# Performance work log

Measured on AMD Instinct MI355X. Metric: run time of the kernel, lower is better.

Reference implementation:

```python
import jax, jax.numpy as jnp
import numpy as np

HEADS = 4
DIM_HEAD = 32
SCALE = DIM_HEAD ** -0.5
GN_EPS = 1e-5


def setup_inputs() -> dict:
    key = jax.random.key(0)
    k1, k2, k3 = jax.random.split(key, 3)
    dim, hidden = 64, HEADS * DIM_HEAD
    x = jax.random.normal(k1, (2, dim, 32, 32, 32), dtype=jnp.float32)
    w_qkv = jax.random.normal(k2, (3 * hidden, dim), dtype=jnp.float32) * (dim ** -0.5)
    w_out = jax.random.normal(k3, (dim, hidden), dtype=jnp.float32) * (hidden ** -0.5)
    b_out = jnp.zeros((dim,), dtype=jnp.float32)
    gn_w = jnp.ones((dim,), dtype=jnp.float32)
    gn_b = jnp.zeros((dim,), dtype=jnp.float32)
    return {"x": x, "w_qkv": w_qkv, "w_out": w_out, "b_out": b_out, "gn_w": gn_w, "gn_b": gn_b}


def reference(x, w_qkv, w_out, b_out, gn_w, gn_b):
    b, c, D, H, W = x.shape
    n = D * H * W
    xf = x.reshape(b, c, n)  # flatten spatial: 1x1 Conv3d == channel matmul
    qkv = jnp.einsum('oc,bcn->bon', w_qkv, xf)  # [b, 3*hidden, n]
    q, k, v = jnp.split(qkv, 3, axis=1)
    rs = lambda t: t.reshape(b, HEADS, DIM_HEAD, n)  # b h d n
    q, k, v = rs(q), rs(k), rs(v)
    q = jax.nn.softmax(q, axis=2) * SCALE   # softmax over head-dim channels
    k = jax.nn.softmax(k, axis=3)           # softmax over spatial positions
    context = jnp.einsum('bhdn,bhen->bhde', k, v)   # [b, h, d, e], tiny
    out = jnp.einsum('bhde,bhdn->bhen', context, q)  # [b, h, e, n]
    out = out.reshape(b, HEADS * DIM_HEAD, n)
    # to_out: 1x1 Conv3d with bias, then GroupNorm(1, dim)
    y = jnp.einsum('oc,bcn->bon', w_out, out) + b_out[None, :, None]
    mean = jnp.mean(y, axis=(1, 2), keepdims=True)
    var = jnp.var(y, axis=(1, 2), keepdims=True)
    y = (y - mean) * jax.lax.rsqrt(var + GN_EPS)
    y = y * gn_w[None, :, None] + gn_b[None, :, None]
    return y.reshape(b, -1, D, H, W)
```

## Files before the change

### kernel.cpp

```cpp
#include <hip/hip_runtime.h>
#include <hip/hip_bf16.h>

#define NB 2
#define C_IN 64
#define N_SP 32768
#define NHEADS 4
#define DH 32
#define HID 128
#define QK_SCALE 0.17677669529663687f
#define GN_EPS_C 1e-5f
#define NGN 2097152.0f

using bf16x8 = __attribute__((ext_vector_type(8))) short;
using f32x4  = __attribute__((ext_vector_type(4))) float;
using u16x4  = __attribute__((ext_vector_type(4))) unsigned short;
using u16x8  = __attribute__((ext_vector_type(8))) unsigned short;

__device__ __forceinline__ unsigned short f2bf(float f) {
    union { float f; unsigned u; } c{f};
    unsigned r = c.u + 0x7FFFu + ((c.u >> 16) & 1u);
    return (unsigned short)(r >> 16);
}
__device__ __forceinline__ float bf2f(unsigned short u) {
    union { unsigned u; float f; } c{ (unsigned)u << 16 };
    return c.f;
}

__device__ __forceinline__ void load_xf(const float* __restrict__ xb, int n0,
        int lg, int lc, bf16x8 xf[4][2]) {
#pragma unroll
    for (int s = 0; s < 4; ++s) {
        int n = n0 + s * 16 + lc;
#pragma unroll
        for (int kk = 0; kk < 2; ++kk) {
            bf16x8 v;
#pragma unroll
            for (int j = 0; j < 8; ++j)
                v[j] = (short)f2bf(xb[(size_t)(kk * 32 + lg * 8 + j) * N_SP + n]);
            xf[s][kk] = v;
        }
    }
}

__global__ __launch_bounds__(256) void kA(const float* __restrict__ x,
        const float* __restrict__ wqkv,
        float* __restrict__ ctx_part, float* __restrict__ ksum_part) {
    __shared__ unsigned short kt[8192];
    __shared__ unsigned short vt[8192];
    const int t = threadIdx.x, wv = t >> 6, l = t & 63, lg = l >> 4, lc = l & 15;
    const int blk = blockIdx.x;
    const int b = blk >> 7, nblk = blk & 127;
    const int n0 = nblk * 256 + wv * 64;

    bf16x8 xf[4][2];
    load_xf(x + (size_t)b * C_IN * N_SP, n0, lg, lc, xf);

    const int di = wv >> 1, ei = wv & 1;
#pragma unroll
    for (int h = 0; h < NHEADS; ++h) {
        f32x4 ka[4][2] = {}, va[4][2] = {};
#pragma unroll
        for (int e = 0; e < 2; ++e)
#pragma unroll
            for (int kk = 0; kk < 2; ++kk) {
                const float* pk = wqkv + (size_t)(HID + h * 32 + e * 16 + lc) * 64 + kk * 32 + lg * 8;
                const float* pv = wqkv + (size_t)(2 * HID + h * 32 + e * 16 + lc) * 64 + kk * 32 + lg * 8;
                bf16x8 wk, wf;
#pragma unroll
                for (int j = 0; j < 8; ++j) { wk[j] = (short)f2bf(pk[j]); wf[j] = (short)f2bf(pv[j]); }
#pragma unroll
                for (int s = 0; s < 4; ++s) {
                    ka[s][e] = __builtin_amdgcn_mfma_f32_16x16x32_bf16(xf[s][kk], wk, ka[s][e], 0, 0, 0);
                    va[s][e] = __builtin_amdgcn_mfma_f32_16x16x32_bf16(xf[s][kk], wf, va[s][e], 0, 0, 0);
                }
            }
        __syncthreads();
#pragma unroll
        for (int s = 0; s < 4; ++s)
#pragma unroll
            for (int e = 0; e < 2; ++e) {
                u16x4 pk, pv;
#pragma unroll
                for (int r = 0; r < 4; ++r) {
                    pk[r] = f2bf(__expf(ka[s][e][r]));
                    pv[r] = f2bf(va[s][e][r]);
                }
                int ch = e * 16 + lc;
                int pos = wv * 64 + s * 16 + lg * 4;
                int ba = (ch * 512 + pos * 2) ^ ((ch & 7) << 4);
                *(u16x4*)((char*)kt + ba) = pk;
                *(u16x4*)((char*)vt + ba) = pv;
            }
        __syncthreads();
        f32x4 ca = {};
        float ks = 0.f;
#pragma unroll
        for (int k0 = 0; k0 < 256; k0 += 32) {
            int ar = di * 16 + lc, br = ei * 16 + lc;
            bf16x8 af = *(const bf16x8*)((const char*)kt + ((ar * 512 + (k0 + lg * 8) * 2) ^ ((ar & 7) << 4)));
            bf16x8 bf = *(const bf16x8*)((const char*)vt + ((br * 512 + (k0 + lg * 8) * 2) ^ ((br & 7) << 4)));
            if (ei == 0) {
#pragma unroll
                for (int j = 0; j < 8; ++j) ks += bf2f((unsigned short)af[j]);
            }
            ca = __builtin_amdgcn_mfma_f32_16x16x32_bf16(af, bf, ca, 0, 0, 0);
        }
        float* cp = ctx_part + ((size_t)(b * 4 + h) * 128 + nblk) * 1024;
#pragma unroll
        for (int r = 0; r < 4; ++r)
            cp[(di * 16 + lg * 4 + r) * 32 + ei * 16 + lc] = ca[r];
        if (ei == 0) {
            ks += __shfl_xor(ks, 16);
            ks += __shfl_xor(ks, 32);
            if (lg == 0)
                ksum_part[((size_t)(b * 4 + h) * 128 + nblk) * 32 + di * 16 + lc] = ks;
        }
    }
}

__global__ __launch_bounds__(256) void kB(const float* __restrict__ ctx_part,
        const float* __restrict__ ksum_part, const float* __restrict__ wout,
        unsigned short* __restrict__ weff) {
    __shared__ float cred2[2][128];
    __shared__ float cred[128];
    __shared__ float ks2[4][32];
    __shared__ float ksl[4];
    const int blk = blockIdx.x;
    const int g = blk >> 3, ds = blk & 7;
    const int bb = g >> 2, h = g & 3;
    const int t = threadIdx.x;
    const int tt = t & 127, th = t >> 7;
    float a = 0.f;
    const float* cp = ctx_part + ((size_t)g * 128 + th * 64) * 1024 + ds * 128 + tt;
#pragma unroll 8
    for (int i = 0; i < 64; ++i) a += cp[(size_t)i * 1024];
    cred2[th][tt] = a;
    if (t < 128) {
        int dl = t >> 5, ic = t & 31;
        float s = 0.f;
        const float* kp = ksum_part + ((size_t)g * 128 + ic * 4) * 32 + ds * 4 + dl;
#pragma unroll
        for (int i = 0; i < 4; ++i) s += kp[i * 32];
        ks2[dl][ic] = s;
    }
    __syncthreads();
    if (t < 128) cred[t] = cred2[0][t] + cred2[1][t];
    if (t < 4) {
        float s = 0.f;
#pragma unroll
        for (int i = 0; i < 32; ++i) s += ks2[t][i];
        ksl[t] = s;
    }
    __syncthreads();
    const int o = t >> 2, dl = t & 3;
    const float* wrow = wout + o * HID + h * 32;
    const float* crow = cred + dl * 32;
    float acc = 0.f;
#pragma unroll
    for (int e = 0; e < 32; ++e) acc = fmaf(wrow[e], crow[e], acc);
    acc /= ksl[dl];
    weff[((size_t)bb * 64 + o) * 128 + h * 32 + ds * 4 + dl] = f2bf(acc);
}

__global__ __launch_bounds__(256) void kC(const float* __restrict__ x,
        const float* __restrict__ wqkv, const unsigned short* __restrict__ weff,
        const float* __restrict__ bout, unsigned short* __restrict__ y_t,
        float* __restrict__ pstats) {
    __shared__ unsigned short qt[256 * 128];
    __shared__ float red[8];
    const int t = threadIdx.x, wv = t >> 6, l = t & 63, lg = l >> 4, lc = l & 15;
    const int blk = blockIdx.x;
    const int b = blk >> 7, nblk = blk & 127;
    const int n0 = nblk * 256 + wv * 64;

    bf16x8 xf[4][2];
    load_xf(x + (size_t)b * C_IN * N_SP, n0, lg, lc, xf);

#pragma unroll
    for (int h = 0; h < NHEADS; ++h) {
        f32x4 qa[2][4] = {};
#pragma unroll
        for (int mi = 0; mi < 2; ++mi)
#pragma unroll
            for (int kk = 0; kk < 2; ++kk) {
                const float* pq = wqkv + (size_t)((h * 2 + mi) * 16 + lc) * 64 + kk * 32 + lg * 8;
                bf16x8 aq;
#pragma unroll
                for (int j = 0; j < 8; ++j) aq[j] = (short)f2bf(pq[j]);
#pragma unroll
                for (int s = 0; s < 4; ++s)
                    qa[mi][s] = __builtin_amdgcn_mfma_f32_16x16x32_bf16(aq, xf[s][kk], qa[mi][s], 0, 0, 0);
            }
#pragma unroll
        for (int s = 0; s < 4; ++s) {
            float m = -1e30f;
#pragma unroll
            for (int mi = 0; mi < 2; ++mi)
#pragma unroll
                for (int r = 0; r < 4; ++r) m = fmaxf(m, qa[mi][s][r]);
            m = fmaxf(m, __shfl_xor(m, 16));
            m = fmaxf(m, __shfl_xor(m, 32));
            float sum = 0.f;
#pragma unroll
            for (int mi = 0; mi < 2; ++mi)
#pragma unroll
                for (int r = 0; r < 4; ++r) {
                    float e = __expf(qa[mi][s][r] - m);
                    qa[mi][s][r] = e; sum += e;
                }
            sum += __shfl_xor(sum, 16);
            sum += __shfl_xor(sum, 32);
            float inv = QK_SCALE / sum;
            int pos = wv * 64 + s * 16 + lc;
            int swz = (pos & 7) << 4;
#pragma unroll
            for (int mi = 0; mi < 2; ++mi) {
                u16x4 pk;
#pragma unroll
                for (int r = 0; r < 4; ++r) pk[r] = f2bf(qa[mi][s][r] * inv);
                int ch0 = h * 32 + mi * 16 + lg * 4;
                *(u16x4*)((char*)qt + ((pos * 256 + ch0 * 2) ^ swz)) = pk;
            }
        }
    }

    f32x4 acc[4][4] = {};
    const unsigned short* wb = weff + (size_t)b * 8192;
#pragma unroll
    for (int kk = 0; kk < 4; ++kk) {
        bf16x8 bq[4];
#pragma unroll
        for (int s = 0; s < 4; ++s) {
            int pos = wv * 64 + s * 16 + lc;
            bq[s] = *(const bf16x8*)((const char*)qt +
                ((pos * 256 + (kk * 32 + lg * 8) * 2) ^ ((pos & 7) << 4)));
        }
#pragma unroll
        for (int mt = 0; mt < 4; ++mt) {
            bf16x8 af = *(const bf16x8*)(wb + (size_t)(mt * 16 + lc) * 128 + kk * 32 + lg * 8);
#pragma unroll
            for (int s = 0; s < 4; ++s)
                acc[mt][s] = __builtin_amdgcn_mfma_f32_16x16x32_bf16(af, bq[s], acc[mt][s], 0, 0, 0);
        }
    }
    float s1 = 0.f, s2 = 0.f;
#pragma unroll
    for (int mt = 0; mt < 4; ++mt) {
        float bo[4];
#pragma unroll
        for (int r = 0; r < 4; ++r) bo[r] = bout[mt * 16 + lg * 4 + r];
#pragma unroll
        for (int s = 0; s < 4; ++s) {
            u16x4 pk;
#pragma unroll
            for (int r = 0; r < 4; ++r) {
                float val = acc[mt][s][r] + bo[r];
                s1 += val;
                s2 = fmaf(val, val, s2);
                pk[r] = f2bf(val);
            }
            int n = nblk * 256 + wv * 64 + s * 16 + lc;
            *(u16x4*)(y_t + ((size_t)b * N_SP + n) * 64 + mt * 16 + lg * 4) = pk;
        }
    }
#pragma unroll
    for (int off = 32; off > 0; off >>= 1) {
        s1 += __shfl_down(s1, off, 64);
        s2 += __shfl_down(s2, off, 64);
    }
    if (l == 0) { red[wv * 2] = s1; red[wv * 2 + 1] = s2; }
    __syncthreads();
    if (t == 0) {
        pstats[blk * 2]     = red[0] + red[2] + red[4] + red[6];
        pstats[blk * 2 + 1] = red[1] + red[3] + red[5] + red[7];
    }
}

__global__ __launch_bounds__(256) void kE(const unsigned short* __restrict__ y_t,
        const float* __restrict__ pstats, const float* __restrict__ gnw,
        const float* __restrict__ gnb, float* __restrict__ out) {
    __shared__ float pr[4];
    __shared__ float ms[2];
    __shared__ float w2s[64], b2s[64];
    const int t = threadIdx.x;
    const int blk = blockIdx.x;
    const int b = blk >> 9, nb = blk & 511;
    float s1 = 0.f, s2 = 0.f;
    if (t < 128) {
        s1 = pstats[(b * 128 + t) * 2];
        s2 = pstats[(b * 128 + t) * 2 + 1];
    }
#pragma unroll
    for (int off = 32; off > 0; off >>= 1) {
        s1 += __shfl_down(s1, off, 64);
        s2 += __shfl_down(s2, off, 64);
    }
    if (t < 128 && (t & 63) == 0) { pr[(t >> 6) * 2] = s1; pr[(t >> 6) * 2 + 1] = s2; }
    __syncthreads();
    if (t == 0) {
        float S1 = pr[0] + pr[2], S2 = pr[1] + pr[3];
        float mean = S1 / NGN;
        float var = S2 / NGN - mean * mean;
        ms[0] = mean; ms[1] = rsqrtf(var + GN_EPS_C);
    }
    __syncthreads();
    if (t < 64) {
        float w2 = gnw[t] * ms[1];
        w2s[t] = w2;
        b2s[t] = gnb[t] - ms[0] * w2;
    }
    __syncthreads();
    const int n = nb * 64 + (t >> 2), o0 = (t & 3) * 16;
    const unsigned short* yp = y_t + ((size_t)b * N_SP + n) * 64 + o0;
    u16x8 v0 = *(const u16x8*)yp;
    u16x8 v1 = *(const u16x8*)(yp + 8);
    float* ob = out + (size_t)b * C_IN * N_SP + n;
#pragma unroll
    for (int j = 0; j < 8; ++j)
        ob[(size_t)(o0 + j) * N_SP] = fmaf(bf2f((unsigned short)v0[j]), w2s[o0 + j], b2s[o0 + j]);
#pragma unroll
    for (int j = 0; j < 8; ++j)
        ob[(size_t)(o0 + 8 + j) * N_SP] = fmaf(bf2f((unsigned short)v1[j]), w2s[o0 + 8 + j], b2s[o0 + 8 + j]);
}

extern "C" void kernel_launch(void* const* d_in, const int* in_sizes, int n_in,
                              void* d_out, int out_size, void* d_ws, size_t ws_size,
                              hipStream_t stream) {
    const float* x    = (const float*)d_in[0];
    const float* wqkv = (const float*)d_in[1];
    const float* wout = (const float*)d_in[2];
    const float* bout = (const float*)d_in[3];
    const float* gnw  = (const float*)d_in[4];
    const float* gnb  = (const float*)d_in[5];
    float* out = (float*)d_out;

    char* ws = (char*)d_ws;
    size_t off = 0;
    float* ctx_part  = (float*)(ws + off); off += (size_t)8 * 128 * 1024 * 4;
    float* ksum_part = (float*)(ws + off); off += (size_t)8 * 128 * 32 * 4;
    unsigned short* weff = (unsigned short*)(ws + off); off += 2 * 8192 * 2;
    unsigned short* y_t  = (unsigned short*)(ws + off); off += (size_t)NB * N_SP * 64 * 2;
    float* pstats = (float*)(ws + off); off += 256 * 2 * 4;

    kA<<<dim3(256), dim3(256), 0, stream>>>(x, wqkv, ctx_part, ksum_part);
    kB<<<dim3(64), dim3(256), 0, stream>>>(ctx_part, ksum_part, wout, weff);
    kC<<<dim3(256), dim3(256), 0, stream>>>(x, wqkv, weff, bout, y_t, pstats);
    kE<<<dim3(1024), dim3(256), 0, stream>>>(y_t, pstats, gnw, gnb, out);
}
```

Baseline: 50.34 us.

## Double threads per block in kA/kC and pre-convert QKV weights to bf16 fragments

Adds a small prep kernel that converts the QKV weights into bf16 MFMA fragment layout once, so kA and kC load ready-made fragments instead of converting fp32 weights per wave. kA and kC now run 512 threads per block, each wave covering 32 positions instead of 64, which halves per-thread register use and adds more waves to hide the latency of the strided x loads. In kA only half the waves take part in the context MFMA, so some waves sit idle there. kE's thread-to-position mapping is also changed so that adjacent threads write adjacent positions, which should coalesce the output stores. The cost is one extra kernel launch.

```diff
diff --git a/kernel.cpp b/kernel.cpp
--- a/kernel.cpp
+++ b/kernel.cpp
@@ -27,9 +27,9 @@
 }
 
 __device__ __forceinline__ void load_xf(const float* __restrict__ xb, int n0,
-        int lg, int lc, bf16x8 xf[4][2]) {
-#pragma unroll
-    for (int s = 0; s < 4; ++s) {
+        int lg, int lc, bf16x8 xf[2][2]) {
+#pragma unroll
+    for (int s = 0; s < 2; ++s) {
         int n = n0 + s * 16 + lc;
 #pragma unroll
         for (int kk = 0; kk < 2; ++kk) {
@@ -42,41 +42,55 @@
     }
 }
 
-__global__ __launch_bounds__(256) void kA(const float* __restrict__ x,
-        const float* __restrict__ wqkv,
+__global__ __launch_bounds__(256) void kprep(const float* __restrict__ wqkv,
+        unsigned short* __restrict__ wfrag) {
+    int t = threadIdx.x;
+#pragma unroll
+    for (int i = 0; i < 12; ++i) {
+        int idx = t + i * 256;
+        int f = idx >> 6, lane = idx & 63;
+        int mt = f >> 1, kk = f & 1;
+        int row = mt * 16 + (lane & 15);
+        int c0 = kk * 32 + (lane >> 4) * 8;
+        const float* wp = wqkv + row * 64 + c0;
+        unsigned short* op = wfrag + (size_t)idx * 8;
+#pragma unroll
+        for (int j = 0; j < 8; ++j) op[j] = f2bf(wp[j]);
+    }
+}
+
+__global__ __launch_bounds__(512) void kA(const float* __restrict__ x,
+        const unsigned short* __restrict__ wfrag,
         float* __restrict__ ctx_part, float* __restrict__ ksum_part) {
     __shared__ unsigned short kt[8192];
     __shared__ unsigned short vt[8192];
     const int t = threadIdx.x, wv = t >> 6, l = t & 63, lg = l >> 4, lc = l & 15;
     const int blk = blockIdx.x;
     const int b = blk >> 7, nblk = blk & 127;
-    const int n0 = nblk * 256 + wv * 64;
-
-    bf16x8 xf[4][2];
+    const int n0 = nblk * 256 + wv * 32;
+
+    bf16x8 xf[2][2];
     load_xf(x + (size_t)b * C_IN * N_SP, n0, lg, lc, xf);
 
-    const int di = wv >> 1, ei = wv & 1;
+    const int di = (wv >> 1) & 1, ei = wv & 1;
 #pragma unroll
     for (int h = 0; h < NHEADS; ++h) {
-        f32x4 ka[4][2] = {}, va[4][2] = {};
+        f32x4 ka[2][2] = {}, va[2][2] = {};
 #pragma unroll
         for (int e = 0; e < 2; ++e)
 #pragma unroll
             for (int kk = 0; kk < 2; ++kk) {
-                const float* pk = wqkv + (size_t)(HID + h * 32 + e * 16 + lc) * 64 + kk * 32 + lg * 8;
-                const float* pv = wqkv + (size_t)(2 * HID + h * 32 + e * 16 + lc) * 64 + kk * 32 + lg * 8;
-                bf16x8 wk, wf;
-#pragma unroll
-                for (int j = 0; j < 8; ++j) { wk[j] = (short)f2bf(pk[j]); wf[j] = (short)f2bf(pv[j]); }
-#pragma unroll
-                for (int s = 0; s < 4; ++s) {
+                bf16x8 wk = *(const bf16x8*)(wfrag + ((size_t)((8 + 2 * h + e) * 2 + kk) * 64 + l) * 8);
+                bf16x8 wf = *(const bf16x8*)(wfrag + ((size_t)((16 + 2 * h + e) * 2 + kk) * 64 + l) * 8);
+#pragma unroll
+                for (int s = 0; s < 2; ++s) {
                     ka[s][e] = __builtin_amdgcn_mfma_f32_16x16x32_bf16(xf[s][kk], wk, ka[s][e], 0, 0, 0);
                     va[s][e] = __builtin_amdgcn_mfma_f32_16x16x32_bf16(xf[s][kk], wf, va[s][e], 0, 0, 0);
                 }
             }
         __syncthreads();
 #pragma unroll
-        for (int s = 0; s < 4; ++s)
+        for (int s = 0; s < 2; ++s)
 #pragma unroll
             for (int e = 0; e < 2; ++e) {
                 u16x4 pk, pv;
@@ -86,34 +100,36 @@
                     pv[r] = f2bf(va[s][e][r]);
                 }
                 int ch = e * 16 + lc;
-                int pos = wv * 64 + s * 16 + lg * 4;
+                int pos = wv * 32 + s * 16 + lg * 4;
                 int ba = (ch * 512 + pos * 2) ^ ((ch & 7) << 4);
                 *(u16x4*)((char*)kt + ba) = pk;
                 *(u16x4*)((char*)vt + ba) = pv;
             }
         __syncthreads();
-        f32x4 ca = {};
-        float ks = 0.f;
-#pragma unroll
-        for (int k0 = 0; k0 < 256; k0 += 32) {
-            int ar = di * 16 + lc, br = ei * 16 + lc;
-            bf16x8 af = *(const bf16x8*)((const char*)kt + ((ar * 512 + (k0 + lg * 8) * 2) ^ ((ar & 7) << 4)));
-            bf16x8 bf = *(const bf16x8*)((const char*)vt + ((br * 512 + (k0 + lg * 8) * 2) ^ ((br & 7) << 4)));
+        if (wv < 4) {
+            f32x4 ca = {};
+            float ks = 0.f;
+#pragma unroll
+            for (int k0 = 0; k0 < 256; k0 += 32) {
+                int ar = di * 16 + lc, br = ei * 16 + lc;
+                bf16x8 af = *(const bf16x8*)((const char*)kt + ((ar * 512 + (k0 + lg * 8) * 2) ^ ((ar & 7) << 4)));
+                bf16x8 bf = *(const bf16x8*)((const char*)vt + ((br * 512 + (k0 + lg * 8) * 2) ^ ((br & 7) << 4)));
+                if (ei == 0) {
+#pragma unroll
+                    for (int j = 0; j < 8; ++j) ks += bf2f((unsigned short)af[j]);
+                }
+                ca = __builtin_amdgcn_mfma_f32_16x16x32_bf16(af, bf, ca, 0, 0, 0);
+            }
+            float* cp = ctx_part + ((size_t)(b * 4 + h) * 128 + nblk) * 1024;
+#pragma unroll
+            for (int r = 0; r < 4; ++r)
+                cp[(di * 16 + lg * 4 + r) * 32 + ei * 16 + lc] = ca[r];
             if (ei == 0) {
-#pragma unroll
-                for (int j = 0; j < 8; ++j) ks += bf2f((unsigned short)af[j]);
-            }
-            ca = __builtin_amdgcn_mfma_f32_16x16x32_bf16(af, bf, ca, 0, 0, 0);
-        }
-        float* cp = ctx_part + ((size_t)(b * 4 + h) * 128 + nblk) * 1024;
-#pragma unroll
-        for (int r = 0; r < 4; ++r)
-            cp[(di * 16 + lg * 4 + r) * 32 + ei * 16 + lc] = ca[r];
-        if (ei == 0) {
-            ks += __shfl_xor(ks, 16);
-            ks += __shfl_xor(ks, 32);
-            if (lg == 0)
-                ksum_part[((size_t)(b * 4 + h) * 128 + nblk) * 32 + di * 16 + lc] = ks;
+                ks += __shfl_xor(ks, 16);
+                ks += __shfl_xor(ks, 32);
+                if (lg == 0)
+                    ksum_part[((size_t)(b * 4 + h) * 128 + nblk) * 32 + di * 16 + lc] = ks;
+            }
         }
     }
 }
@@ -162,37 +178,34 @@
     weff[((size_t)bb * 64 + o) * 128 + h * 32 + ds * 4 + dl] = f2bf(acc);
 }
 
-__global__ __launch_bounds__(256) void kC(const float* __restrict__ x,
-        const float* __restrict__ wqkv, const unsigned short* __restrict__ weff,
+__global__ __launch_bounds__(512) void kC(const float* __restrict__ x,
+        const unsigned short* __restrict__ wfrag, const unsigned short* __restrict__ weff,
         const float* __restrict__ bout, unsigned short* __restrict__ y_t,
         float* __restrict__ pstats) {
     __shared__ unsigned short qt[256 * 128];
-    __shared__ float red[8];
+    __shared__ float red[16];
     const int t = threadIdx.x, wv = t >> 6, l = t & 63, lg = l >> 4, lc = l & 15;
     const int blk = blockIdx.x;
     const int b = blk >> 7, nblk = blk & 127;
-    const int n0 = nblk * 256 + wv * 64;
-
-    bf16x8 xf[4][2];
+    const int n0 = nblk * 256 + wv * 32;
+
+    bf16x8 xf[2][2];
     load_xf(x + (size_t)b * C_IN * N_SP, n0, lg, lc, xf);
 
 #pragma unroll
     for (int h = 0; h < NHEADS; ++h) {
-        f32x4 qa[2][4] = {};
+        f32x4 qa[2][2] = {};
 #pragma unroll
         for (int mi = 0; mi < 2; ++mi)
 #pragma unroll
             for (int kk = 0; kk < 2; ++kk) {
-                const float* pq = wqkv + (size_t)((h * 2 + mi) * 16 + lc) * 64 + kk * 32 + lg * 8;
-                bf16x8 aq;
-#pragma unroll
-                for (int j = 0; j < 8; ++j) aq[j] = (short)f2bf(pq[j]);
-#pragma unroll
-                for (int s = 0; s < 4; ++s)
+                bf16x8 aq = *(const bf16x8*)(wfrag + ((size_t)((h * 2 + mi) * 2 + kk) * 64 + l) * 8);
+#pragma unroll
+                for (int s = 0; s < 2; ++s)
                     qa[mi][s] = __builtin_amdgcn_mfma_f32_16x16x32_bf16(aq, xf[s][kk], qa[mi][s], 0, 0, 0);
             }
 #pragma unroll
-        for (int s = 0; s < 4; ++s) {
+        for (int s = 0; s < 2; ++s) {
             float m = -1e30f;
 #pragma unroll
             for (int mi = 0; mi < 2; ++mi)
@@ -211,7 +224,7 @@
             sum += __shfl_xor(sum, 16);
             sum += __shfl_xor(sum, 32);
             float inv = QK_SCALE / sum;
-            int pos = wv * 64 + s * 16 + lc;
+            int pos = wv * 32 + s * 16 + lc;
             int swz = (pos & 7) << 4;
 #pragma unroll
             for (int mi = 0; mi < 2; ++mi) {
@@ -224,14 +237,14 @@
         }
     }
 
-    f32x4 acc[4][4] = {};
+    f32x4 acc[4][2] = {};
     const unsigned short* wb = weff + (size_t)b * 8192;
 #pragma unroll
     for (int kk = 0; kk < 4; ++kk) {
-        bf16x8 bq[4];
-#pragma unroll
-        for (int s = 0; s < 4; ++s) {
-            int pos = wv * 64 + s * 16 + lc;
+        bf16x8 bq[2];
+#pragma unroll
+        for (int s = 0; s < 2; ++s) {
+            int pos = wv * 32 + s * 16 + lc;
             bq[s] = *(const bf16x8*)((const char*)qt +
                 ((pos * 256 + (kk * 32 + lg * 8) * 2) ^ ((pos & 7) << 4)));
         }
@@ -239,7 +252,7 @@
         for (int mt = 0; mt < 4; ++mt) {
             bf16x8 af = *(const bf16x8*)(wb + (size_t)(mt * 16 + lc) * 128 + kk * 32 + lg * 8);
 #pragma unroll
-            for (int s = 0; s < 4; ++s)
+            for (int s = 0; s < 2; ++s)
                 acc[mt][s] = __builtin_amdgcn_mfma_f32_16x16x32_bf16(af, bq[s], acc[mt][s], 0, 0, 0);
         }
     }
@@ -250,7 +263,7 @@
 #pragma unroll
         for (int r = 0; r < 4; ++r) bo[r] = bout[mt * 16 + lg * 4 + r];
 #pragma unroll
-        for (int s = 0; s < 4; ++s) {
+        for (int s = 0; s < 2; ++s) {
             u16x4 pk;
 #pragma unroll
             for (int r = 0; r < 4; ++r) {
@@ -259,7 +272,7 @@
                 s2 = fmaf(val, val, s2);
                 pk[r] = f2bf(val);
             }
-            int n = nblk * 256 + wv * 64 + s * 16 + lc;
+            int n = n0 + s * 16 + lc;
             *(u16x4*)(y_t + ((size_t)b * N_SP + n) * 64 + mt * 16 + lg * 4) = pk;
         }
     }
@@ -271,15 +284,18 @@
     if (l == 0) { red[wv * 2] = s1; red[wv * 2 + 1] = s2; }
     __syncthreads();
     if (t == 0) {
-        pstats[blk * 2]     = red[0] + red[2] + red[4] + red[6];
-        pstats[blk * 2 + 1] = red[1] + red[3] + red[5] + red[7];
+        float S1 = 0.f, S2 = 0.f;
+#pragma unroll
+        for (int w = 0; w < 8; ++w) { S1 += red[w * 2]; S2 += red[w * 2 + 1]; }
+        pstats[(b * 128 + nblk) * 2]     = S1;
+        pstats[(b * 128 + nblk) * 2 + 1] = S2;
     }
 }
 
 __global__ __launch_bounds__(256) void kE(const unsigned short* __restrict__ y_t,
         const float* __restrict__ pstats, const float* __restrict__ gnw,
         const float* __restrict__ gnb, float* __restrict__ out) {
-    __shared__ float pr[4];
+    __shared__ float red[4];
     __shared__ float ms[2];
     __shared__ float w2s[64], b2s[64];
     const int t = threadIdx.x;
@@ -295,10 +311,10 @@
         s1 += __shfl_down(s1, off, 64);
         s2 += __shfl_down(s2, off, 64);
     }
-    if (t < 128 && (t & 63) == 0) { pr[(t >> 6) * 2] = s1; pr[(t >> 6) * 2 + 1] = s2; }
+    if (t < 128 && (t & 63) == 0) { red[(t >> 6) * 2] = s1; red[(t >> 6) * 2 + 1] = s2; }
     __syncthreads();
     if (t == 0) {
-        float S1 = pr[0] + pr[2], S2 = pr[1] + pr[3];
+        float S1 = red[0] + red[2], S2 = red[1] + red[3];
         float mean = S1 / NGN;
         float var = S2 / NGN - mean * mean;
         ms[0] = mean; ms[1] = rsqrtf(var + GN_EPS_C);
@@ -310,7 +326,7 @@
         b2s[t] = gnb[t] - ms[0] * w2;
     }
     __syncthreads();
-    const int n = nb * 64 + (t >> 2), o0 = (t & 3) * 16;
+    const int n = nb * 64 + (t & 63), o0 = (t >> 6) * 16;
     const unsigned short* yp = y_t + ((size_t)b * N_SP + n) * 64 + o0;
     u16x8 v0 = *(const u16x8*)yp;
     u16x8 v1 = *(const u16x8*)(yp + 8);
@@ -336,14 +352,16 @@
 
     char* ws = (char*)d_ws;
     size_t off = 0;
+    unsigned short* wfrag = (unsigned short*)(ws + off); off += 49152;
     float* ctx_part  = (float*)(ws + off); off += (size_t)8 * 128 * 1024 * 4;
     float* ksum_part = (float*)(ws + off); off += (size_t)8 * 128 * 32 * 4;
     unsigned short* weff = (unsigned short*)(ws + off); off += 2 * 8192 * 2;
     unsigned short* y_t  = (unsigned short*)(ws + off); off += (size_t)NB * N_SP * 64 * 2;
-    float* pstats = (float*)(ws + off); off += 256 * 2 * 4;
-
-    kA<<<dim3(256), dim3(256), 0, stream>>>(x, wqkv, ctx_part, ksum_part);
+    float* pstats = (float*)(ws + off); off += NB * 128 * 2 * 4;
+
+    kprep<<<dim3(1), dim3(256), 0, stream>>>(wqkv, wfrag);
+    kA<<<dim3(256), dim3(512), 0, stream>>>(x, wfrag, ctx_part, ksum_part);
     kB<<<dim3(64), dim3(256), 0, stream>>>(ctx_part, ksum_part, wout, weff);
-    kC<<<dim3(256), dim3(256), 0, stream>>>(x, wqkv, weff, bout, y_t, pstats);
+    kC<<<dim3(256), dim3(512), 0, stream>>>(x, wfrag, weff, bout, y_t, pstats);
     kE<<<dim3(1024), dim3(256), 0, stream>>>(y_t, pstats, gnw, gnb, out);
 }
```

Result: faster. 47.30 us (-6.0%).
